# Performance work log

Measured on AMD Instinct MI355X. Metric: run time of the kernel, lower is better.

The kernel has to match this reference:

```python
import jax, jax.numpy as jnp
import numpy as np

LN_EPS = 1e-5  # torch LayerNorm default

def _phi(x):
    # elu(x) + 1 feature map
    return jax.nn.elu(x) + 1.0

def setup_inputs() -> dict:
    key = jax.random.key(0)
    ks = jax.random.split(key, 5)
    B, N, D = 4, 8192, 1024
    s = 1.0 / np.sqrt(D)
    return {
        "H": jax.random.normal(ks[0], (B, N, D), dtype=jnp.float32),
        "W_qkv": jax.random.normal(ks[1], (3 * D, D), dtype=jnp.float32) * s,
        "b_qkv": jax.random.normal(ks[2], (3 * D,), dtype=jnp.float32) * 0.01,
        "W_proj": jax.random.normal(ks[3], (D, D), dtype=jnp.float32) * s,
        "b_proj": jax.random.normal(ks[4], (D,), dtype=jnp.float32) * 0.01,
        "gamma": jnp.ones((D,), dtype=jnp.float32),
        "beta": jnp.zeros((D,), dtype=jnp.float32),
    }

def reference(H, W_qkv, b_qkv, W_proj, b_proj, gamma, beta):
    B, N, D = H.shape
    num_heads = 16
    head_dim = D // num_heads
    residual = H
    # qkv projection: (B,N,3D)
    qkv = jnp.einsum('bnd,ed->bne', H, W_qkv) + b_qkv
    qkv = qkv.reshape(B, N, 3, num_heads, head_dim).transpose(2, 0, 3, 1, 4)
    q, k, v = qkv[0], qkv[1], qkv[2]  # each (B,h,N,d)
    q = _phi(q)
    k = _phi(k)
    # kv outer-product accumulated over nodes: (B,h,d,v)
    kv = jnp.einsum('bhnd,bhnv->bhdv', k, v)
    k1 = k.sum(axis=2)  # (B,h,d)
    qkv_out = jnp.einsum('bhnd,bhdv->bhnv', q, kv)
    qk1 = jnp.sum(q * k1[:, :, None, :], axis=-1, keepdims=True)
    out = qkv_out / jnp.clip(qk1, 1e-6, None)
    # NOTE: faithful to original -- reshape (B,h,N,d) -> (B,N,D) WITHOUT head transpose
    out = out.reshape(B, N, D)
    out = jnp.einsum('bnd,ed->bne', out, W_proj) + b_proj
    # LayerNorm over last dim
    mu = out.mean(axis=-1, keepdims=True)
    var = out.var(axis=-1, keepdims=True)
    out = (out - mu) * jax.lax.rsqrt(var + LN_EPS) * gamma + beta
    # dropout is identity at inference
    return out + residual
```

## Files before the change

kernel.cpp:

```cpp
#include <hip/hip_runtime.h>


typedef __attribute__((ext_vector_type(4))) float f32x4;
typedef __attribute__((ext_vector_type(8))) short bf16x8;

__device__ __forceinline__ unsigned short f2b(float f) {
    unsigned u = __float_as_uint(f);
    u = (u + 0x7FFFu + ((u >> 16) & 1u)) >> 16;
    return (unsigned short)u;
}
__device__ __forceinline__ float b2f(unsigned short h) {
    return __uint_as_float(((unsigned)h) << 16);
}

__device__ __forceinline__ void glds16(const void* gp, void* lp) {
    __builtin_amdgcn_global_load_lds(
        (__attribute__((address_space(1))) void*)(unsigned long long)gp,
        (__attribute__((address_space(3))) void*)(unsigned int)(unsigned long long)lp,
        16, 0, 0);
}

__global__ __launch_bounds__(256) void cvt_all(const float* __restrict__ H,
                                               const float* __restrict__ Wq,
                                               const float* __restrict__ Wp,
                                               unsigned short* __restrict__ hbf,
                                               unsigned short* __restrict__ wqb,
                                               unsigned short* __restrict__ wpb) {
    const int blk = blockIdx.x;
    const float* src; unsigned short* dst; long n4; int b0, nb;
    if (blk < 1792)      { src = H;  dst = hbf; n4 = 8388608; b0 = 0;    nb = 1792; }
    else if (blk < 1920) { src = Wq; dst = wqb; n4 = 786432;  b0 = 1792; nb = 128; }
    else                 { src = Wp; dst = wpb; n4 = 262144;  b0 = 1920; nb = 64; }
    long i = (long)(blk - b0) * 256 + threadIdx.x;
    const long stride = (long)nb * 256;
    for (; i < n4; i += stride) {
        float4 v = ((const float4*)src)[i];
        ushort4 o;
        o.x = f2b(v.x); o.y = f2b(v.y); o.z = f2b(v.z); o.w = f2b(v.w);
        ((ushort4*)dst)[i] = o;
    }
}

template<int MODE>
__global__ __launch_bounds__(512) void gemm256(const unsigned short* __restrict__ A,
                                               const unsigned short* __restrict__ B,
                                               const float* __restrict__ bias,
                                               void* __restrict__ Cout,
                                               int mb, int N, int K) {
    __shared__ unsigned short lds[2][2][256][64];
    const int tid = threadIdx.x;
    const int wid = tid >> 6, lane = tid & 63;
    const int wr = wid >> 2, wc = wid & 3;
    const int lr = lane & 15, lq = lane >> 4;
    const int cpx = (int)gridDim.x >> 3;
    const int L = ((int)blockIdx.x & 7) * cpx + ((int)blockIdx.x >> 3);
    const int nbv = N >> 8;
    const int gsz = 4 * nbv;
    const int g = L / gsz, r = L % gsz;
    const int bn = r >> 2;
    const int bm = g * 4 + (r & 3);
    const size_t aRow0 = (size_t)bm * 256, bRow0 = (size_t)bn * 256;

    const int sr8 = lane >> 3;
    const int ssw = ((lane & 7) ^ sr8) * 8;
    const unsigned short* aG = A + (aRow0 + (size_t)(wid * 8 + sr8)) * K + ssw;
    const unsigned short* bG = B + (bRow0 + (size_t)(wid * 8 + sr8)) * K + ssw;

    f32x4 acc[8][4] = {};
    const char* base = (const char*)&lds[0][0][0][0];

    auto stage = [&](int buf, int k0) {
#pragma unroll
        for (int j = 0; j < 8; ++j) {
            const unsigned short* g2 = (j < 4 ? aG : bG) + (size_t)(j & 3) * 64 * K + k0;
            glds16(g2, &lds[buf][j >> 2][(j & 3) * 64 + wid * 8][0]);
        }
    };
    auto ldA = [&](int cur, int mi, int ks) {
        int row = wr * 128 + mi * 16 + lr;
        int off = (cur * 2 + 0) * 32768 + row * 128 + ((((ks << 2) | lq) ^ (row & 7)) << 4);
        return *(const bf16x8*)(base + off);
    };
    auto ldB = [&](int cur, int ni, int ks) {
        int row = wc * 64 + ni * 16 + lr;
        int off = (cur * 2 + 1) * 32768 + row * 128 + ((((ks << 2) | lq) ^ (row & 7)) << 4);
        return *(const bf16x8*)(base + off);
    };

    const int nt = K >> 6;
    stage(0, 0);
    asm volatile("s_waitcnt vmcnt(0)" ::: "memory");
    __builtin_amdgcn_s_barrier();

    bf16x8 af[4][2], bfr[4][2];
    for (int t = 0; t < nt; ++t) {
        const int cur = t & 1;
#pragma unroll
        for (int mi = 0; mi < 4; ++mi) {
            af[mi][0] = ldA(cur, mi, 0); af[mi][1] = ldA(cur, mi, 1);
        }
#pragma unroll
        for (int ni = 0; ni < 2; ++ni) {
            bfr[ni][0] = ldB(cur, ni, 0); bfr[ni][1] = ldB(cur, ni, 1);
        }
        if (t + 1 < nt) stage(cur ^ 1, (t + 1) << 6);
        __builtin_amdgcn_s_barrier();
        __builtin_amdgcn_s_setprio(1);
#pragma unroll
        for (int mi = 0; mi < 4; ++mi)
#pragma unroll
            for (int ni = 0; ni < 2; ++ni)
#pragma unroll
                for (int ks = 0; ks < 2; ++ks)
                    acc[mi][ni] = __builtin_amdgcn_mfma_f32_16x16x32_bf16(
                        af[mi][ks], bfr[ni][ks], acc[mi][ni], 0, 0, 0);
        __builtin_amdgcn_s_setprio(0);
        __builtin_amdgcn_s_barrier();
#pragma unroll
        for (int ni = 2; ni < 4; ++ni) {
            bfr[ni][0] = ldB(cur, ni, 0); bfr[ni][1] = ldB(cur, ni, 1);
        }
        __builtin_amdgcn_s_barrier();
        __builtin_amdgcn_s_setprio(1);
#pragma unroll
        for (int mi = 0; mi < 4; ++mi)
#pragma unroll
            for (int ni = 2; ni < 4; ++ni)
#pragma unroll
                for (int ks = 0; ks < 2; ++ks)
                    acc[mi][ni] = __builtin_amdgcn_mfma_f32_16x16x32_bf16(
                        af[mi][ks], bfr[ni][ks], acc[mi][ni], 0, 0, 0);
        __builtin_amdgcn_s_setprio(0);
        __builtin_amdgcn_s_barrier();
#pragma unroll
        for (int mi = 0; mi < 4; ++mi) {
            af[mi][0] = ldA(cur, mi + 4, 0); af[mi][1] = ldA(cur, mi + 4, 1);
        }
        __builtin_amdgcn_s_barrier();
        __builtin_amdgcn_s_setprio(1);
#pragma unroll
        for (int mi = 0; mi < 4; ++mi)
#pragma unroll
            for (int ni = 2; ni < 4; ++ni)
#pragma unroll
                for (int ks = 0; ks < 2; ++ks)
                    acc[mi + 4][ni] = __builtin_amdgcn_mfma_f32_16x16x32_bf16(
                        af[mi][ks], bfr[ni][ks], acc[mi + 4][ni], 0, 0, 0);
        __builtin_amdgcn_s_setprio(0);
        __builtin_amdgcn_s_barrier();
        __builtin_amdgcn_s_setprio(1);
#pragma unroll
        for (int mi = 0; mi < 4; ++mi)
#pragma unroll
            for (int ni = 0; ni < 2; ++ni)
#pragma unroll
                for (int ks = 0; ks < 2; ++ks)
                    acc[mi + 4][ni] = __builtin_amdgcn_mfma_f32_16x16x32_bf16(
                        af[mi][ks], bfr[ni][ks], acc[mi + 4][ni], 0, 0, 0);
        __builtin_amdgcn_s_setprio(0);
        asm volatile("s_waitcnt vmcnt(0)" ::: "memory");
        __builtin_amdgcn_s_barrier();
        __builtin_amdgcn_sched_barrier(0);
    }
#pragma unroll
    for (int mi = 0; mi < 8; ++mi) {
#pragma unroll
        for (int ni = 0; ni < 4; ++ni) {
            int col = (int)bRow0 + wc * 64 + ni * 16 + lr;
            float bv = bias[col];
#pragma unroll
            for (int r2 = 0; r2 < 4; ++r2) {
                size_t row = aRow0 + wr * 128 + mi * 16 + lq * 4 + r2;
                float v = acc[mi][ni][r2] + bv;
                if (MODE == 0) {
                    if (col < 2048) v = (v > 0.f) ? (v + 1.f) : __expf(v);
                }
                ((unsigned short*)Cout)[row * (size_t)N + col] = f2b(v);
            }
        }
    }
}

__global__ __launch_bounds__(256) void kv_partial(const unsigned short* __restrict__ qkv,
                                                  float* __restrict__ part) {
    const int bh = blockIdx.x, chunk = blockIdx.y;
    const int b = bh >> 4, h = bh & 15;
    __shared__ unsigned short kb[16][64];
    __shared__ unsigned short vb[16][64];
    const int tid = threadIdx.x;
    const int d0 = (tid >> 4) * 4, v0 = (tid & 15) * 4;
    float acc[4][4] = {};
    float k1a[4] = {0.f, 0.f, 0.f, 0.f};
    const size_t base = ((size_t)b * 8192 + (size_t)chunk * 1024) * 3072;
    const int nn = tid >> 4;
    const int which = (tid >> 3) & 1;
    const int cg = tid & 7;
    const size_t loff = base + (size_t)nn * 3072 + (which ? 2048 : 1024) + h * 64 + cg * 8;

    for (int n0 = 0; n0 < 1024; n0 += 16) {
        uint4 val = *(const uint4*)(qkv + loff + (size_t)n0 * 3072);
        if (which) *(uint4*)(&vb[nn][cg * 8]) = val;
        else       *(uint4*)(&kb[nn][cg * 8]) = val;
        __syncthreads();
#pragma unroll 4
        for (int j = 0; j < 16; ++j) {
            ushort4 ku = *(const ushort4*)(&kb[j][d0]);
            ushort4 vu = *(const ushort4*)(&vb[j][v0]);
            float kd[4] = {b2f(ku.x), b2f(ku.y), b2f(ku.z), b2f(ku.w)};
            float vd[4] = {b2f(vu.x), b2f(vu.y), b2f(vu.z), b2f(vu.w)};
#pragma unroll
            for (int i = 0; i < 4; ++i)
#pragma unroll
                for (int jj = 0; jj < 4; ++jj)
                    acc[i][jj] += kd[i] * vd[jj];
            if ((tid & 15) == 0)
#pragma unroll
                for (int i = 0; i < 4; ++i) k1a[i] += kd[i];
        }
        __syncthreads();
    }
    float* dst = part + ((size_t)bh * 8 + chunk) * 4160;
#pragma unroll
    for (int i = 0; i < 4; ++i)
#pragma unroll
        for (int jj = 0; jj < 4; ++jj)
            dst[(d0 + i) * 64 + v0 + jj] = acc[i][jj];
    if ((tid & 15) == 0)
#pragma unroll
        for (int i = 0; i < 4; ++i) dst[4096 + d0 + i] = k1a[i];
}

__global__ __launch_bounds__(256) void apply_attn(const unsigned short* __restrict__ qkv,
                                                  const float* __restrict__ part,
                                                  unsigned short* __restrict__ att) {
    const int nblk = blockIdx.x;
    const int bh = blockIdx.y;
    const int b = bh >> 4, h = bh & 15;
    __shared__ float kvs[64][64];
    __shared__ float k1s[64];
    const float* src = part + (size_t)bh * 8 * 4160;
    for (int i = threadIdx.x; i < 4096; i += 256) {
        float s = 0.f;
#pragma unroll
        for (int c = 0; c < 8; ++c) s += src[c * 4160 + i];
        kvs[i >> 6][i & 63] = s;
    }
    if (threadIdx.x < 64) {
        float s = 0.f;
#pragma unroll
        for (int c = 0; c < 8; ++c) s += src[c * 4160 + 4096 + threadIdx.x];
        k1s[threadIdx.x] = s;
    }
    __syncthreads();
    const int t = threadIdx.x;
    const int r = t >> 2, qt = t & 3;
    const int n = nblk * 64 + r;
    const unsigned short* qrow = qkv + ((size_t)b * 8192 + n) * 3072 + h * 64;
    float acc[16] = {};
    float qk1 = 0.f;
    for (int dc = 0; dc < 64; dc += 8) {
        uint4 qu = *(const uint4*)(qrow + dc);
        unsigned qw[4] = {qu.x, qu.y, qu.z, qu.w};
#pragma unroll
        for (int jj = 0; jj < 8; ++jj) {
            float qd = (jj & 1) ? __uint_as_float(qw[jj >> 1] & 0xFFFF0000u)
                                : __uint_as_float(qw[jj >> 1] << 16);
            int d = dc + jj;
            qk1 += qd * k1s[d];
            const float4* kr = (const float4*)(&kvs[d][qt * 16]);
            float4 c0 = kr[0], c1 = kr[1], c2 = kr[2], c3 = kr[3];
            acc[0]  += qd * c0.x; acc[1]  += qd * c0.y; acc[2]  += qd * c0.z; acc[3]  += qd * c0.w;
            acc[4]  += qd * c1.x; acc[5]  += qd * c1.y; acc[6]  += qd * c1.z; acc[7]  += qd * c1.w;
            acc[8]  += qd * c2.x; acc[9]  += qd * c2.y; acc[10] += qd * c2.z; acc[11] += qd * c2.w;
            acc[12] += qd * c3.x; acc[13] += qd * c3.y; acc[14] += qd * c3.z; acc[15] += qd * c3.w;
        }
    }
    float rinv = 1.f / fmaxf(qk1, 1e-6f);
    union { unsigned short us[16]; uint4 u4[2]; } ob;
#pragma unroll
    for (int j = 0; j < 16; ++j) ob.us[j] = f2b(acc[j] * rinv);
    unsigned short* dst = att + (((size_t)b * 8192) + h * 512 + (n >> 4)) * 1024
                              + (n & 15) * 64 + qt * 16;
    *(uint4*)dst = ob.u4[0];
    *(uint4*)(dst + 8) = ob.u4[1];
}

__global__ __launch_bounds__(256) void ln_residual(const unsigned short* __restrict__ X,
                                                   const float* __restrict__ H,
                                                   const float* __restrict__ gamma,
                                                   const float* __restrict__ beta,
                                                   float* __restrict__ out,
                                                   int nrows) {
    const int lane = threadIdx.x & 63;
    int row = blockIdx.x * 4 + (threadIdx.x >> 6);
    const int rstride = gridDim.x * 4;
    for (; row < nrows; row += rstride) {
        const unsigned short* x = X + (size_t)row * 1024;
        float v[16];
        float s = 0.f, s2 = 0.f;
#pragma unroll
        for (int j = 0; j < 4; ++j) {
            ushort4 u = *(const ushort4*)(x + j * 256 + lane * 4);
            float a = b2f(u.x), b = b2f(u.y), c = b2f(u.z), d = b2f(u.w);
            v[j * 4 + 0] = a; v[j * 4 + 1] = b; v[j * 4 + 2] = c; v[j * 4 + 3] = d;
            s += a + b + c + d;
            s2 += a * a + b * b + c * c + d * d;
        }
#pragma unroll
        for (int o = 32; o > 0; o >>= 1) {
            s  += __shfl_xor(s, o, 64);
            s2 += __shfl_xor(s2, o, 64);
        }
        const float mu = s * (1.f / 1024.f);
        const float var = s2 * (1.f / 1024.f) - mu * mu;
        const float inv = rsqrtf(var + 1e-5f);
        const float* hrow = H + (size_t)row * 1024;
        float* orow = out + (size_t)row * 1024;
#pragma unroll
        for (int j = 0; j < 4; ++j) {
            const int c = j * 256 + lane * 4;
            float4 g = *(const float4*)(gamma + c);
            float4 bt = *(const float4*)(beta + c);
            float4 hr = *(const float4*)(hrow + c);
            float4 o;
            o.x = (v[j * 4 + 0] - mu) * inv * g.x + bt.x + hr.x;
            o.y = (v[j * 4 + 1] - mu) * inv * g.y + bt.y + hr.y;
            o.z = (v[j * 4 + 2] - mu) * inv * g.z + bt.z + hr.z;
            o.w = (v[j * 4 + 3] - mu) * inv * g.w + bt.w + hr.w;
            *(float4*)(orow + c) = o;
        }
    }
}

extern "C" void kernel_launch(void* const* d_in, const int* in_sizes, int n_in,
                              void* d_out, int out_size, void* d_ws, size_t ws_size,
                              hipStream_t stream) {
    const float* H     = (const float*)d_in[0];
    const float* Wqkv  = (const float*)d_in[1];
    const float* bqkv  = (const float*)d_in[2];
    const float* Wproj = (const float*)d_in[3];
    const float* bproj = (const float*)d_in[4];
    const float* gamma = (const float*)d_in[5];
    const float* beta  = (const float*)d_in[6];
    float* out = (float*)d_out;
    char* ws = (char*)d_ws;

    unsigned short* wq_bf = (unsigned short*)(ws);
    unsigned short* wp_bf = (unsigned short*)(ws + 6291456);
    unsigned short* hbf   = (unsigned short*)(ws + 8388608);
    unsigned short* att   = hbf;
    unsigned short* qkvbf = (unsigned short*)(ws + 75497472);
    unsigned short* out2  = (unsigned short*)(ws + 75497472);
    float*          part  = (float*)(ws + 277889024);

    cvt_all<<<1984, 256, 0, stream>>>(H, Wqkv, Wproj, hbf, wq_bf, wp_bf);

    gemm256<0><<<1536, 512, 0, stream>>>(hbf, wq_bf, bqkv, (void*)qkvbf,
                                         128, 3072, 1024);

    kv_partial<<<dim3(64, 8), 256, 0, stream>>>(qkvbf, part);

    apply_attn<<<dim3(128, 64), 256, 0, stream>>>(qkvbf, part, att);

    gemm256<1><<<512, 512, 0, stream>>>(att, wp_bf, bproj, (void*)out2,
                                        128, 1024, 1024);

    ln_residual<<<2048, 256, 0, stream>>>(out2, H, gamma, beta, out, 32768);
}
```

Before: 612.0 us.

## Use MFMA for attention apply with bf16 KV and separate reduction kernel

Adds a kv_finish kernel that reduces the per-chunk KV partials once per head into a transposed bf16 matrix plus an fp32 k1 vector, instead of every apply_attn block redoing the 8-way reduction. apply_attn now loads the bf16 KV into XOR-swizzled shared memory, computes the q·k1 normaliser separately, and performs q·KV with 16x16x32 bf16 MFMA instructions rather than scalar FMAs. This removes redundant partial-sum work and moves the matmul onto matrix cores. The cost is an extra launch and rounding KV to bf16, plus narrower 2-byte scattered output stores.

```diff
diff --git a/kernel.cpp b/kernel.cpp
--- a/kernel.cpp
+++ b/kernel.cpp
@@ -224,65 +224,96 @@
     for (int i = 0; i < 4; ++i)
 #pragma unroll
         for (int jj = 0; jj < 4; ++jj)
-            dst[(d0 + i) * 64 + v0 + jj] = acc[i][jj];
+            dst[(v0 + jj) * 64 + d0 + i] = acc[i][jj];
     if ((tid & 15) == 0)
 #pragma unroll
         for (int i = 0; i < 4; ++i) dst[4096 + d0 + i] = k1a[i];
 }
 
+__global__ __launch_bounds__(256) void kv_finish(const float* __restrict__ part,
+                                                 unsigned short* __restrict__ kvbf,
+                                                 float* __restrict__ k1f) {
+    const int bh = blockIdx.x;
+    const float* src = part + (size_t)bh * 8 * 4160;
+    for (int i = threadIdx.x; i < 4096; i += 256) {
+        float s = 0.f;
+#pragma unroll
+        for (int c = 0; c < 8; ++c) s += src[c * 4160 + i];
+        kvbf[(size_t)bh * 4096 + i] = f2b(s);
+    }
+    if (threadIdx.x < 64) {
+        float s = 0.f;
+#pragma unroll
+        for (int c = 0; c < 8; ++c) s += src[c * 4160 + 4096 + threadIdx.x];
+        k1f[bh * 64 + threadIdx.x] = s;
+    }
+}
+
 __global__ __launch_bounds__(256) void apply_attn(const unsigned short* __restrict__ qkv,
-                                                  const float* __restrict__ part,
+                                                  const unsigned short* __restrict__ kvbf,
+                                                  const float* __restrict__ k1f,
                                                   unsigned short* __restrict__ att) {
     const int nblk = blockIdx.x;
     const int bh = blockIdx.y;
     const int b = bh >> 4, h = bh & 15;
-    __shared__ float kvs[64][64];
+    __shared__ unsigned short kvs[64][64];
     __shared__ float k1s[64];
-    const float* src = part + (size_t)bh * 8 * 4160;
-    for (int i = threadIdx.x; i < 4096; i += 256) {
+    __shared__ float qk1s[64];
+    const int tid = threadIdx.x;
+    {
+        const int v = tid >> 3, s = tid & 7;
+        const uint4* srcv = (const uint4*)(kvbf + (size_t)bh * 4096);
+#pragma unroll
+        for (int half = 0; half < 2; ++half) {
+            int vv = v + half * 32;
+            uint4 val = srcv[vv * 8 + s];
+            *(uint4*)(&kvs[vv][(s ^ (vv & 7)) * 8]) = val;
+        }
+        if (tid < 64) k1s[tid] = k1f[bh * 64 + tid];
+    }
+    __syncthreads();
+    const int n0 = nblk * 64;
+    const size_t qbase = ((size_t)b * 8192 + n0) * 3072 + h * 64;
+    {
+        const int row = tid >> 2, dq = (tid & 3) * 16;
+        const unsigned short* qp = qkv + qbase + (size_t)row * 3072 + dq;
         float s = 0.f;
 #pragma unroll
-        for (int c = 0; c < 8; ++c) s += src[c * 4160 + i];
-        kvs[i >> 6][i & 63] = s;
-    }
-    if (threadIdx.x < 64) {
-        float s = 0.f;
-#pragma unroll
-        for (int c = 0; c < 8; ++c) s += src[c * 4160 + 4096 + threadIdx.x];
-        k1s[threadIdx.x] = s;
+        for (int g2 = 0; g2 < 2; ++g2) {
+            ushort4 u0 = *(const ushort4*)(qp + g2 * 8);
+            ushort4 u1 = *(const ushort4*)(qp + g2 * 8 + 4);
+            const float* kp = &k1s[dq + g2 * 8];
+            s += b2f(u0.x) * kp[0] + b2f(u0.y) * kp[1] + b2f(u0.z) * kp[2] + b2f(u0.w) * kp[3]
+               + b2f(u1.x) * kp[4] + b2f(u1.y) * kp[5] + b2f(u1.z) * kp[6] + b2f(u1.w) * kp[7];
+        }
+        s += __shfl_xor(s, 1, 64);
+        s += __shfl_xor(s, 2, 64);
+        if ((tid & 3) == 0) qk1s[row] = s;
     }
     __syncthreads();
-    const int t = threadIdx.x;
-    const int r = t >> 2, qt = t & 3;
-    const int n = nblk * 64 + r;
-    const unsigned short* qrow = qkv + ((size_t)b * 8192 + n) * 3072 + h * 64;
-    float acc[16] = {};
-    float qk1 = 0.f;
-    for (int dc = 0; dc < 64; dc += 8) {
-        uint4 qu = *(const uint4*)(qrow + dc);
-        unsigned qw[4] = {qu.x, qu.y, qu.z, qu.w};
-#pragma unroll
-        for (int jj = 0; jj < 8; ++jj) {
-            float qd = (jj & 1) ? __uint_as_float(qw[jj >> 1] & 0xFFFF0000u)
-                                : __uint_as_float(qw[jj >> 1] << 16);
-            int d = dc + jj;
-            qk1 += qd * k1s[d];
-            const float4* kr = (const float4*)(&kvs[d][qt * 16]);
-            float4 c0 = kr[0], c1 = kr[1], c2 = kr[2], c3 = kr[3];
-            acc[0]  += qd * c0.x; acc[1]  += qd * c0.y; acc[2]  += qd * c0.z; acc[3]  += qd * c0.w;
-            acc[4]  += qd * c1.x; acc[5]  += qd * c1.y; acc[6]  += qd * c1.z; acc[7]  += qd * c1.w;
-            acc[8]  += qd * c2.x; acc[9]  += qd * c2.y; acc[10] += qd * c2.z; acc[11] += qd * c2.w;
-            acc[12] += qd * c3.x; acc[13] += qd * c3.y; acc[14] += qd * c3.z; acc[15] += qd * c3.w;
-        }
-    }
-    float rinv = 1.f / fmaxf(qk1, 1e-6f);
-    union { unsigned short us[16]; uint4 u4[2]; } ob;
-#pragma unroll
-    for (int j = 0; j < 16; ++j) ob.us[j] = f2b(acc[j] * rinv);
-    unsigned short* dst = att + (((size_t)b * 8192) + h * 512 + (n >> 4)) * 1024
-                              + (n & 15) * 64 + qt * 16;
-    *(uint4*)dst = ob.u4[0];
-    *(uint4*)(dst + 8) = ob.u4[1];
+    const int w = tid >> 6, lane = tid & 63;
+    const int lr = lane & 15, lq = lane >> 4;
+    bf16x8 af[2];
+#pragma unroll
+    for (int ks = 0; ks < 2; ++ks)
+        af[ks] = *(const bf16x8*)(qkv + qbase + (size_t)(w * 16 + lr) * 3072 + ks * 32 + lq * 8);
+    f32x4 acc[4] = {};
+#pragma unroll
+    for (int ni = 0; ni < 4; ++ni)
+#pragma unroll
+        for (int ks = 0; ks < 2; ++ks) {
+            int v = ni * 16 + lr;
+            bf16x8 bf = *(const bf16x8*)(&kvs[v][(((ks << 2) | lq) ^ (v & 7)) * 8]);
+            acc[ni] = __builtin_amdgcn_mfma_f32_16x16x32_bf16(af[ks], bf, acc[ni], 0, 0, 0);
+        }
+    unsigned short* dstrow = att + (((size_t)b * 8192) + h * 512 + nblk * 4 + w) * 1024;
+#pragma unroll
+    for (int r = 0; r < 4; ++r) {
+        float rinv = 1.f / fmaxf(qk1s[w * 16 + lq * 4 + r], 1e-6f);
+#pragma unroll
+        for (int ni = 0; ni < 4; ++ni)
+            dstrow[(lq * 4 + r) * 64 + ni * 16 + lr] = f2b(acc[ni][r] * rinv);
+    }
 }
 
 __global__ __launch_bounds__(256) void ln_residual(const unsigned short* __restrict__ X,
@@ -351,6 +382,8 @@
     unsigned short* att   = hbf;
     unsigned short* qkvbf = (unsigned short*)(ws + 75497472);
     unsigned short* out2  = (unsigned short*)(ws + 75497472);
+    unsigned short* kvbf  = (unsigned short*)(ws + 276824064);
+    float*          k1f   = (float*)(ws + 277348352);
     float*          part  = (float*)(ws + 277889024);
 
     cvt_all<<<1984, 256, 0, stream>>>(H, Wqkv, Wproj, hbf, wq_bf, wp_bf);
@@ -359,8 +392,9 @@
                                          128, 3072, 1024);
 
     kv_partial<<<dim3(64, 8), 256, 0, stream>>>(qkvbf, part);
-
-    apply_attn<<<dim3(128, 64), 256, 0, stream>>>(qkvbf, part, att);
+    kv_finish<<<64, 256, 0, stream>>>(part, kvbf, k1f);
+
+    apply_attn<<<dim3(128, 64), 256, 0, stream>>>(qkvbf, kvbf, k1f, att);
 
     gemm256<1><<<512, 512, 0, stream>>>(att, wp_bf, bproj, (void*)out2,
                                         128, 1024, 1024);
```

Measured after the change: 564.0 us. 1.09x faster.
